# Performance work log

Measured on AMD Instinct MI355X. Metric: run time of the kernel, lower is better.

The kernel has to match this reference:

```python
import jax, jax.numpy as jnp
import numpy as np

WS = (14, 14)
NUM_HEADS = 12
DIM = 768
HEAD_DIM = DIM // NUM_HEADS
N_TOK = WS[0] * WS[1] + 1  # 197 (cls token)
NUM_REL = (2 * WS[0] - 1) * (2 * WS[1] - 1) + 3  # 732
B = 64


def _build_rel_pos_index():
    ch, cw = np.arange(WS[0]), np.arange(WS[1])
    coords = np.stack(np.meshgrid(ch, cw, indexing='ij'))  # [2,h,w]
    cf = coords.reshape(2, -1)  # [2, h*w]
    rel = cf[:, :, None] - cf[:, None, :]  # [2, hw, hw]
    rel = rel.transpose(1, 2, 0).astype(np.int64)
    rel[:, :, 0] += WS[0] - 1
    rel[:, :, 1] += WS[1] - 1
    rel[:, :, 0] *= 2 * WS[1] - 1
    idx = np.zeros((N_TOK, N_TOK), dtype=np.int64)
    idx[1:, 1:] = rel.sum(-1)
    idx[0, 0:] = NUM_REL - 3
    idx[0:, 0] = NUM_REL - 2
    idx[0, 0] = NUM_REL - 1
    return idx.astype(np.int32)


def setup_inputs() -> dict:
    key = jax.random.key(0)
    ks = jax.random.split(key, 7)
    s = 0.02
    return {
        'x': jax.random.normal(ks[0], (B, N_TOK, DIM), jnp.float32),
        'qkv_w': jax.random.normal(ks[1], (3 * DIM, DIM), jnp.float32) * s,
        'q_bias': jax.random.normal(ks[2], (DIM,), jnp.float32) * s,
        'v_bias': jax.random.normal(ks[3], (DIM,), jnp.float32) * s,
        'rpb_table': jax.random.normal(ks[4], (NUM_REL, NUM_HEADS), jnp.float32) * s,
        'proj_w': jax.random.normal(ks[5], (DIM, DIM), jnp.float32) * s,
        'proj_b': jax.random.normal(ks[6], (DIM,), jnp.float32) * s,
        'rel_pos_index': jnp.asarray(_build_rel_pos_index()),
    }


def reference(x, qkv_w, q_bias, v_bias, rpb_table, proj_w, proj_b, rel_pos_index):
    Bb, N, C = x.shape
    scale = HEAD_DIM ** -0.5
    # qkv bias: [q_bias, zeros(k), v_bias]
    qkv_bias = jnp.concatenate([q_bias, jnp.zeros_like(v_bias), v_bias])
    qkv = x @ qkv_w.T + qkv_bias  # [B,N,3C]
    qkv = qkv.reshape(Bb, N, 3, NUM_HEADS, HEAD_DIM).transpose(2, 0, 3, 1, 4)
    q, k, v = qkv[0], qkv[1], qkv[2]  # [B,H,N,hd]
    attn = jnp.einsum('bhnd,bhmd->bhnm', q * scale, k)
    # gather relative position bias: [N,N,H] -> [1,H,N,N]
    rpb = rpb_table[rel_pos_index]  # [N,N,H]
    attn = attn + rpb.transpose(2, 0, 1)[None]
    attn = jax.nn.softmax(attn, axis=-1)
    out = jnp.einsum('bhnm,bhmd->bhnd', attn, v)
    out = out.transpose(0, 2, 1, 3).reshape(Bb, N, NUM_HEADS * HEAD_DIM)
    return out @ proj_w.T + proj_b
```

## Files before the change

### kernel.cpp

```cpp
#include <hip/hip_runtime.h>
#include <hip/hip_bf16.h>
#include <cstdint>
#include <cstddef>

typedef __bf16 bf16x8 __attribute__((ext_vector_type(8)));
typedef float f32x4 __attribute__((ext_vector_type(4)));

#define DI __device__ __forceinline__
#define AS1 __attribute__((address_space(1)))
#define AS3 __attribute__((address_space(3)))

DI unsigned short f2bf(float x) {
    union { float f; unsigned int u; } v; v.f = x;
    unsigned int u = v.u;
    u += 0x7FFFu + ((u >> 16) & 1u);
    return (unsigned short)(u >> 16);
}

#define BATCH 64
#define NH 12
#define NTOK 197
#define NTOK_P 208
#define HD 64
#define DIM 768
#define MROWS 12608
#define MPAD 224
#define PLDS 232
#define CPAD 132
#define QSCALE 0.18033688f
#define LOG2E 1.4426950408889634f

DI int xcd_swz(int orig, int nwg) {
    int q = nwg >> 3, r = nwg & 7;
    int x = orig & 7, l = orig >> 3;
    return (x < r ? x * (q + 1) : r * (q + 1) + (x - r) * q) + l;
}

DI int swz(int row, int col_elem) {
    return (row * 64 + col_elem) ^ ((row & 7) << 3);
}


__global__ void cvt3_bf16_kernel(const float* __restrict__ a, unsigned short* __restrict__ oa, int na4,
                                 const float* __restrict__ b, unsigned short* __restrict__ ob, int nb4,
                                 const float* __restrict__ c, unsigned short* __restrict__ oc, int nc4) {
    int i = blockIdx.x * blockDim.x + threadIdx.x;
    const float* src; unsigned short* dst; int k;
    if (i < na4) { src = a; dst = oa; k = i; }
    else if (i < na4 + nb4) { src = b; dst = ob; k = i - na4; }
    else if (i < na4 + nb4 + nc4) { src = c; dst = oc; k = i - na4 - nb4; }
    else return;
    float4 f = ((const float4*)src)[k];
    ushort4 o;
    o.x = f2bf(f.x); o.y = f2bf(f.y); o.z = f2bf(f.z); o.w = f2bf(f.w);
    ((ushort4*)dst)[k] = o;
}

__global__ void build_rpb2_kernel(const float* __restrict__ table, const int* __restrict__ idx,
                                  float* __restrict__ out) {
    int i = blockIdx.x * blockDim.x + threadIdx.x;
    if (i >= NH * 13 * 13 * 256) return;
    int j = i & 3;
    int lane = (i >> 2) & 63;
    int t = (i >> 8) % 13;
    int qt = ((i >> 8) / 13) % 13;
    int h = (i >> 8) / 169;
    int row = qt * 16 + ((lane >> 4) << 2) + j;
    int col = t * 16 + (lane & 15);
    float v = 0.f;
    if (row < NTOK && col < NTOK) v = table[idx[row * NTOK + col] * NH + h] * LOG2E;
    out[i] = v;
}

__global__ void zero_vt_pad_kernel(unsigned short* __restrict__ vt) {
    const int npad = MPAD - NTOK;
    int i = blockIdx.x * blockDim.x + threadIdx.x;
    if (i >= BATCH * NH * HD * npad) return;
    int c = NTOK + (i % npad);
    int row = i / npad;
    vt[(size_t)row * MPAD + c] = 0;
}


template<int EPI>
__launch_bounds__(256)
__global__ void gemm_bt_kernel(const unsigned short* __restrict__ A,
                               const unsigned short* __restrict__ W,
                               const float* __restrict__ bias0,
                               const float* __restrict__ bias1,
                               void* __restrict__ out0,
                               unsigned short* __restrict__ out1,
                               unsigned short* __restrict__ out2,
                               int M, int ntiles)
{
    __shared__ __align__(16) unsigned short smem[32768];
    const int K = DIM;
    const int NT = K / 64;
    int wgid = xcd_swz(blockIdx.x, gridDim.x);
    int mt = wgid / ntiles, nt = wgid % ntiles;
    int m0 = mt * 128, n0 = nt * 128;
    int tid = threadIdx.x;
    int lane = tid & 63, w = tid >> 6;
    int wr = (w >> 1) * 64, wc = (w & 1) * 64;

    const int st_row = lane >> 3;
    const int st_col = ((lane & 7) ^ (lane >> 3)) << 3;

    f32x4 acc[4][4] = {};

    auto stage = [&](int buf, int ks) {
        unsigned short* as = smem + buf * 8192;
        unsigned short* bs = smem + 16384 + buf * 8192;
#pragma unroll
        for (int i = 0; i < 4; i++) {
            int s = w * 4 + i;
            int arow = m0 + s * 8 + st_row; if (arow >= M) arow = M - 1;
            __builtin_amdgcn_global_load_lds(
                (const AS1 void*)(A + (size_t)arow * K + ks + st_col),
                (AS3 void*)(as + s * 512), 16, 0, 0);
        }
#pragma unroll
        for (int i = 0; i < 4; i++) {
            int s = w * 4 + i;
            __builtin_amdgcn_global_load_lds(
                (const AS1 void*)(W + (size_t)(n0 + s * 8 + st_row) * K + ks + st_col),
                (AS3 void*)(bs + s * 512), 16, 0, 0);
        }
    };

    stage(0, 0);
    __syncthreads();
    int cur = 0;
    for (int t = 0; t < NT; ++t) {
        if (t + 1 < NT) stage(cur ^ 1, (t + 1) * 64);
        const unsigned short* as = smem + cur * 8192;
        const unsigned short* bs = smem + 16384 + cur * 8192;
#pragma unroll
        for (int kc = 0; kc < 2; kc++) {
            bf16x8 af[4], bfr[4];
#pragma unroll
            for (int x = 0; x < 4; x++)
                af[x] = *(const bf16x8*)&as[swz(wr + x * 16 + (lane & 15), kc * 32 + (lane >> 4) * 8)];
#pragma unroll
            for (int y = 0; y < 4; y++)
                bfr[y] = *(const bf16x8*)&bs[swz(wc + y * 16 + (lane & 15), kc * 32 + (lane >> 4) * 8)];
#pragma unroll
            for (int x = 0; x < 4; x++)
#pragma unroll
                for (int y = 0; y < 4; y++)
                    acc[x][y] = __builtin_amdgcn_mfma_f32_16x16x32_bf16(af[x], bfr[y], acc[x][y], 0, 0, 0);
        }
        __syncthreads();
        cur ^= 1;
    }

    if constexpr (EPI == 1) {
#pragma unroll
        for (int x = 0; x < 4; x++)
#pragma unroll
            for (int y = 0; y < 4; y++)
#pragma unroll
                for (int j = 0; j < 4; j++) {
                    int m = m0 + wr + x * 16 + (lane >> 4) * 4 + j;
                    int n = n0 + wc + y * 16 + (lane & 15);
                    if (m < M)
                        ((float*)out0)[(size_t)m * DIM + n] = acc[x][y][j] + bias0[n];
                }
    } else {
        int which = n0 / DIM;
        int hn0 = n0 - which * DIM;
        unsigned short* lc = smem;

#pragma unroll
        for (int x = 0; x < 4; x++)
#pragma unroll
            for (int y = 0; y < 4; y++)
#pragma unroll
                for (int j = 0; j < 4; j++) {
                    int ml = wr + x * 16 + (lane >> 4) * 4 + j;
                    int nl = wc + y * 16 + (lane & 15);
                    float val = acc[x][y][j];
                    if (which == 0) val = (val + bias0[hn0 + nl]) * QSCALE;
                    else if (which == 2) val = val + bias1[hn0 + nl];
                    lc[ml * CPAD + nl] = f2bf(val);
                }
        __syncthreads();

        if (which != 2) {
            unsigned short* outq = (which == 0) ? (unsigned short*)out0 : out1;
            int c4 = (lane & 31) * 4;
            int h = (hn0 >> 6) + (c4 >> 6), d = c4 & 63;
            for (int it = 0; it < 16; ++it) {
                int r = it * 8 + w * 2 + (lane >> 5);
                int m = m0 + r;
                if (m >= M) continue;
                int b = m / NTOK, t = m - b * NTOK;
                ushort4 q4 = *(const ushort4*)&lc[r * CPAD + c4];
                *(ushort4*)&outq[(((size_t)b * NH + h) * NTOK_P + t) * HD + d] = q4;
            }
        } else {
            int mh = w >> 1, hs = w & 1;
            int h = (hn0 >> 6) + hs;
            int ml = mh * 64 + lane;
            int m = m0 + ml;
            if (m < M) {
                int b = m / NTOK, t = m - b * NTOK;
                unsigned short* vbase = out2 + (((size_t)b * NH + h) * HD) * MPAD + t;
#pragma unroll 8
                for (int d = 0; d < 64; ++d)
                    vbase[(size_t)d * MPAD] = lc[ml * CPAD + hs * 64 + d];
            }
        }
    }
}


__launch_bounds__(64)
__global__ void attn_kernel(const unsigned short* __restrict__ qbuf,
                            const unsigned short* __restrict__ kbuf,
                            const unsigned short* __restrict__ vt,
                            const float* __restrict__ rpb2,
                            unsigned short* __restrict__ ao)
{
    __shared__ __align__(16) unsigned short p_lds[16][PLDS];
    int bid = xcd_swz(blockIdx.x, gridDim.x);
    int qt = bid % 13, bh = bid / 13;
    int b = bh / NH, h = bh - b * NH;
    int lane = threadIdx.x;
    int r0 = qt * 16;
    int col_l = lane & 15, hi = lane >> 4;

    {
        int rr = lane >> 2, cc = NTOK_P + (lane & 3) * 4;
        ushort4 z = {0, 0, 0, 0};
        *(ushort4*)&p_lds[rr][cc] = z;
    }

    const size_t kqbase = (size_t)bh * NTOK_P * HD;
    int qrow = r0 + col_l;
    bf16x8 qf0 = *(const bf16x8*)&qbuf[kqbase + (size_t)qrow * HD + hi * 8];
    bf16x8 qf1 = *(const bf16x8*)&qbuf[kqbase + (size_t)qrow * HD + 32 + hi * 8];

    const float* rpbase = rpb2 + (((size_t)(h * 13 + qt) * 13) << 8) + (lane << 2);

    float lrow[4] = {0.f, 0.f, 0.f, 0.f};
#pragma unroll
    for (int t = 0; t < 13; t++) {
        int krow = t * 16 + col_l;
        bf16x8 kf0 = *(const bf16x8*)&kbuf[kqbase + (size_t)krow * HD + hi * 8];
        bf16x8 kf1 = *(const bf16x8*)&kbuf[kqbase + (size_t)krow * HD + 32 + hi * 8];
        f32x4 z = {0.f, 0.f, 0.f, 0.f};
        f32x4 a = __builtin_amdgcn_mfma_f32_16x16x32_bf16(qf0, kf0, z, 0, 0, 0);
        f32x4 s = __builtin_amdgcn_mfma_f32_16x16x32_bf16(qf1, kf1, a, 0, 0, 0);
        float4 rb = *(const float4*)&rpbase[t << 8];
        float rbj[4] = {rb.x, rb.y, rb.z, rb.w};
        bool masked = (t * 16 + col_l >= NTOK);
#pragma unroll
        for (int j = 0; j < 4; j++) {
            float v = s[j] + rbj[j];
            if (masked) v = -1e30f;
            float p = exp2f(v);
            lrow[j] += p;
            p_lds[hi * 4 + j][t * 16 + col_l] = f2bf(p);
        }
    }
#pragma unroll
    for (int j = 0; j < 4; j++) {
        float lv = lrow[j];
        lv += __shfl_xor(lv, 1);
        lv += __shfl_xor(lv, 2);
        lv += __shfl_xor(lv, 4);
        lv += __shfl_xor(lv, 8);
        lrow[j] = lv;
    }
    float inv[4];
#pragma unroll
    for (int j = 0; j < 4; j++)
        inv[j] = __builtin_amdgcn_rcpf(lrow[j]);

    f32x4 o[4] = {};
    const size_t vbase = (size_t)bh * HD * MPAD;
    __builtin_amdgcn_s_setprio(1);
#pragma unroll
    for (int c = 0; c < 7; c++) {
        bf16x8 pf = *(const bf16x8*)&p_lds[col_l][c * 32 + hi * 8];
#pragma unroll
        for (int n = 0; n < 4; n++) {
            bf16x8 vf = *(const bf16x8*)&vt[vbase + (size_t)(n * 16 + col_l) * MPAD + c * 32 + hi * 8];
            o[n] = __builtin_amdgcn_mfma_f32_16x16x32_bf16(pf, vf, o[n], 0, 0, 0);
        }
    }
    __builtin_amdgcn_s_setprio(0);

    int rbase = r0 + hi * 4;
#pragma unroll
    for (int n = 0; n < 4; n++)
#pragma unroll
        for (int j = 0; j < 4; j++) {
            int tok = rbase + j;
            if (tok < NTOK) {
                float val = o[n][j] * inv[j];
                ao[((size_t)b * NTOK + tok) * DIM + h * HD + n * 16 + col_l] = f2bf(val);
            }
        }
}


extern "C" void kernel_launch(void* const* d_in, const int* in_sizes, int n_in,
                              void* d_out, int out_size, void* d_ws, size_t ws_size,
                              hipStream_t stream)
{
    const float* x      = (const float*)d_in[0];
    const float* qkv_w  = (const float*)d_in[1];
    const float* q_bias = (const float*)d_in[2];
    const float* v_bias = (const float*)d_in[3];
    const float* rpb_t  = (const float*)d_in[4];
    const float* proj_w = (const float*)d_in[5];
    const float* proj_b = (const float*)d_in[6];
    const int*   relidx = (const int*)d_in[7];
    float* out = (float*)d_out;

    char* ws = (char*)d_ws;
    const size_t SZ_XBF  = (size_t)MROWS * DIM * 2;
    const size_t SZ_QKVW = (size_t)3 * DIM * DIM * 2;
    const size_t SZ_PRJW = (size_t)DIM * DIM * 2;
    const size_t SZ_QK   = (size_t)BATCH * NH * NTOK_P * HD * 2;
    const size_t SZ_VT   = (size_t)BATCH * NH * HD * MPAD * 2;

    unsigned short* x_bf = (unsigned short*)ws;
    unsigned short* ao   = x_bf;
    size_t off = SZ_XBF;
    unsigned short* qkvw_bf  = (unsigned short*)(ws + off); off += SZ_QKVW;
    unsigned short* projw_bf = (unsigned short*)(ws + off); off += SZ_PRJW;
    unsigned short* qbuf     = (unsigned short*)(ws + off); off += SZ_QK;
    unsigned short* kbuf     = (unsigned short*)(ws + off); off += SZ_QK;
    unsigned short* vtbuf    = (unsigned short*)(ws + off); off += SZ_VT;
    float* rpbf              = (float*)(ws + off);

    const int NA4 = MROWS * DIM / 4, NB4 = 3 * DIM * DIM / 4, NC4 = DIM * DIM / 4;
    cvt3_bf16_kernel<<<(NA4 + NB4 + NC4 + 255) / 256, 256, 0, stream>>>(
        x, x_bf, NA4, qkv_w, qkvw_bf, NB4, proj_w, projw_bf, NC4);
    build_rpb2_kernel<<<(NH * 13 * 13 * 256 + 255) / 256, 256, 0, stream>>>(rpb_t, relidx, rpbf);
    zero_vt_pad_kernel<<<(BATCH * NH * HD * (MPAD - NTOK) + 255) / 256, 256, 0, stream>>>(vtbuf);

    gemm_bt_kernel<0><<<99 * 18, 256, 0, stream>>>(x_bf, qkvw_bf, q_bias, v_bias,
                                                   (void*)qbuf, kbuf, vtbuf, MROWS, 18);
    attn_kernel<<<BATCH * NH * 13, 64, 0, stream>>>(qbuf, kbuf, vtbuf, rpbf, ao);
    gemm_bt_kernel<1><<<99 * 6, 256, 0, stream>>>(ao, projw_bf, proj_b, nullptr,
                                                  (void*)out, nullptr, nullptr, MROWS, 6);
    (void)in_sizes; (void)n_in; (void)out_size; (void)ws_size;
}
```

Baseline: 194.1 us.

## Process two 16-row query tiles per attention wave to reuse K/V loads

Each attention block now handles 32 query rows (two 16-row MFMA groups) instead of 16, so each K and V fragment loaded from global memory feeds two MFMAs. The grid shrinks from 13 to 7 query tiles per head, and the relative-position-bias layout and its build kernel are reorganized to match. The goal is to halve redundant K/V global traffic and per-block overhead, at the cost of more registers and LDS per wave, fewer blocks, and some wasted work on the clamped last tile (rows 208–223).

Result: faster. 185.3 us (-4.5%).

```diff
diff --git a/kernel.cpp b/kernel.cpp
--- a/kernel.cpp
+++ b/kernel.cpp
@@ -25,7 +25,7 @@
 #define DIM 768
 #define MROWS 12608
 #define MPAD 224
-#define PLDS 232
+#define PLDS2 236
 #define CPAD 132
 #define QSCALE 0.18033688f
 #define LOG2E 1.4426950408889634f
@@ -59,13 +59,15 @@
 __global__ void build_rpb2_kernel(const float* __restrict__ table, const int* __restrict__ idx,
                                   float* __restrict__ out) {
     int i = blockIdx.x * blockDim.x + threadIdx.x;
-    if (i >= NH * 13 * 13 * 256) return;
+    if (i >= NH * 7 * 13 * 512) return;
     int j = i & 3;
-    int lane = (i >> 2) & 63;
-    int t = (i >> 8) % 13;
-    int qt = ((i >> 8) / 13) % 13;
-    int h = (i >> 8) / 169;
-    int row = qt * 16 + ((lane >> 4) << 2) + j;
+    int g = (i >> 2) & 1;
+    int lane = (i >> 3) & 63;
+    int rest = i >> 9;
+    int t = rest % 13;
+    int qt = (rest / 13) % 7;
+    int h = rest / 91;
+    int row = qt * 32 + g * 16 + ((lane >> 4) << 2) + j;
     int col = t * 16 + (lane & 15);
     float v = 0.f;
     if (row < NTOK && col < NTOK) v = table[idx[row * NTOK + col] * NH + h] * LOG2E;
@@ -222,87 +224,101 @@
                             const float* __restrict__ rpb2,
                             unsigned short* __restrict__ ao)
 {
-    __shared__ __align__(16) unsigned short p_lds[16][PLDS];
+    __shared__ __align__(16) unsigned short p_lds[32][PLDS2];
     int bid = xcd_swz(blockIdx.x, gridDim.x);
-    int qt = bid % 13, bh = bid / 13;
+    int qt = bid % 7, bh = bid / 7;
     int b = bh / NH, h = bh - b * NH;
     int lane = threadIdx.x;
-    int r0 = qt * 16;
+    int r0 = qt * 32;
     int col_l = lane & 15, hi = lane >> 4;
 
     {
-        int rr = lane >> 2, cc = NTOK_P + (lane & 3) * 4;
+        int rr = lane >> 1, cc = NTOK_P + (lane & 1) * 8;
         ushort4 z = {0, 0, 0, 0};
         *(ushort4*)&p_lds[rr][cc] = z;
+        *(ushort4*)&p_lds[rr][cc + 4] = z;
     }
 
     const size_t kqbase = (size_t)bh * NTOK_P * HD;
-    int qrow = r0 + col_l;
-    bf16x8 qf0 = *(const bf16x8*)&qbuf[kqbase + (size_t)qrow * HD + hi * 8];
-    bf16x8 qf1 = *(const bf16x8*)&qbuf[kqbase + (size_t)qrow * HD + 32 + hi * 8];
-
-    const float* rpbase = rpb2 + (((size_t)(h * 13 + qt) * 13) << 8) + (lane << 2);
-
-    float lrow[4] = {0.f, 0.f, 0.f, 0.f};
+    int qr0 = r0 + col_l;      if (qr0 > NTOK_P - 1) qr0 = NTOK_P - 1;
+    int qr1 = r0 + 16 + col_l; if (qr1 > NTOK_P - 1) qr1 = NTOK_P - 1;
+    bf16x8 qf0a = *(const bf16x8*)&qbuf[kqbase + (size_t)qr0 * HD + hi * 8];
+    bf16x8 qf0b = *(const bf16x8*)&qbuf[kqbase + (size_t)qr0 * HD + 32 + hi * 8];
+    bf16x8 qf1a = *(const bf16x8*)&qbuf[kqbase + (size_t)qr1 * HD + hi * 8];
+    bf16x8 qf1b = *(const bf16x8*)&qbuf[kqbase + (size_t)qr1 * HD + 32 + hi * 8];
+
+    const float* rpbase = rpb2 + ((size_t)(h * 7 + qt) * 13) * 512 + lane * 8;
+
+    float lrow[2][4] = {};
 #pragma unroll
     for (int t = 0; t < 13; t++) {
         int krow = t * 16 + col_l;
         bf16x8 kf0 = *(const bf16x8*)&kbuf[kqbase + (size_t)krow * HD + hi * 8];
         bf16x8 kf1 = *(const bf16x8*)&kbuf[kqbase + (size_t)krow * HD + 32 + hi * 8];
         f32x4 z = {0.f, 0.f, 0.f, 0.f};
-        f32x4 a = __builtin_amdgcn_mfma_f32_16x16x32_bf16(qf0, kf0, z, 0, 0, 0);
-        f32x4 s = __builtin_amdgcn_mfma_f32_16x16x32_bf16(qf1, kf1, a, 0, 0, 0);
-        float4 rb = *(const float4*)&rpbase[t << 8];
+        f32x4 sA = __builtin_amdgcn_mfma_f32_16x16x32_bf16(qf0a, kf0, z, 0, 0, 0);
+        sA = __builtin_amdgcn_mfma_f32_16x16x32_bf16(qf0b, kf1, sA, 0, 0, 0);
+        f32x4 sB = __builtin_amdgcn_mfma_f32_16x16x32_bf16(qf1a, kf0, z, 0, 0, 0);
+        sB = __builtin_amdgcn_mfma_f32_16x16x32_bf16(qf1b, kf1, sB, 0, 0, 0);
+        float4 ra = *(const float4*)&rpbase[(size_t)t * 512];
+        float4 rb = *(const float4*)&rpbase[(size_t)t * 512 + 4];
+        float raj[4] = {ra.x, ra.y, ra.z, ra.w};
         float rbj[4] = {rb.x, rb.y, rb.z, rb.w};
         bool masked = (t * 16 + col_l >= NTOK);
 #pragma unroll
         for (int j = 0; j < 4; j++) {
-            float v = s[j] + rbj[j];
-            if (masked) v = -1e30f;
-            float p = exp2f(v);
-            lrow[j] += p;
-            p_lds[hi * 4 + j][t * 16 + col_l] = f2bf(p);
-        }
-    }
-#pragma unroll
-    for (int j = 0; j < 4; j++) {
-        float lv = lrow[j];
-        lv += __shfl_xor(lv, 1);
-        lv += __shfl_xor(lv, 2);
-        lv += __shfl_xor(lv, 4);
-        lv += __shfl_xor(lv, 8);
-        lrow[j] = lv;
-    }
-    float inv[4];
-#pragma unroll
-    for (int j = 0; j < 4; j++)
-        inv[j] = __builtin_amdgcn_rcpf(lrow[j]);
-
-    f32x4 o[4] = {};
+            float vA = sA[j] + raj[j];
+            float vB = sB[j] + rbj[j];
+            if (masked) { vA = -1e30f; vB = -1e30f; }
+            float pA = exp2f(vA);
+            float pB = exp2f(vB);
+            lrow[0][j] += pA;
+            lrow[1][j] += pB;
+            p_lds[hi * 4 + j][t * 16 + col_l] = f2bf(pA);
+            p_lds[16 + hi * 4 + j][t * 16 + col_l] = f2bf(pB);
+        }
+    }
+    float inv[2][4];
+#pragma unroll
+    for (int g = 0; g < 2; g++)
+#pragma unroll
+        for (int j = 0; j < 4; j++) {
+            float lv = lrow[g][j];
+            lv += __shfl_xor(lv, 1);
+            lv += __shfl_xor(lv, 2);
+            lv += __shfl_xor(lv, 4);
+            lv += __shfl_xor(lv, 8);
+            inv[g][j] = __builtin_amdgcn_rcpf(lv);
+        }
+
+    f32x4 o[2][4] = {};
     const size_t vbase = (size_t)bh * HD * MPAD;
     __builtin_amdgcn_s_setprio(1);
 #pragma unroll
     for (int c = 0; c < 7; c++) {
-        bf16x8 pf = *(const bf16x8*)&p_lds[col_l][c * 32 + hi * 8];
+        bf16x8 pf0 = *(const bf16x8*)&p_lds[col_l][c * 32 + hi * 8];
+        bf16x8 pf1 = *(const bf16x8*)&p_lds[16 + col_l][c * 32 + hi * 8];
 #pragma unroll
         for (int n = 0; n < 4; n++) {
             bf16x8 vf = *(const bf16x8*)&vt[vbase + (size_t)(n * 16 + col_l) * MPAD + c * 32 + hi * 8];
-            o[n] = __builtin_amdgcn_mfma_f32_16x16x32_bf16(pf, vf, o[n], 0, 0, 0);
+            o[0][n] = __builtin_amdgcn_mfma_f32_16x16x32_bf16(pf0, vf, o[0][n], 0, 0, 0);
+            o[1][n] = __builtin_amdgcn_mfma_f32_16x16x32_bf16(pf1, vf, o[1][n], 0, 0, 0);
         }
     }
     __builtin_amdgcn_s_setprio(0);
 
-    int rbase = r0 + hi * 4;
-#pragma unroll
-    for (int n = 0; n < 4; n++)
-#pragma unroll
-        for (int j = 0; j < 4; j++) {
-            int tok = rbase + j;
-            if (tok < NTOK) {
-                float val = o[n][j] * inv[j];
-                ao[((size_t)b * NTOK + tok) * DIM + h * HD + n * 16 + col_l] = f2bf(val);
+#pragma unroll
+    for (int g = 0; g < 2; g++)
+#pragma unroll
+        for (int n = 0; n < 4; n++)
+#pragma unroll
+            for (int j = 0; j < 4; j++) {
+                int tok = r0 + g * 16 + hi * 4 + j;
+                if (tok < NTOK) {
+                    float val = o[g][n][j] * inv[g][j];
+                    ao[((size_t)b * NTOK + tok) * DIM + h * HD + n * 16 + col_l] = f2bf(val);
+                }
             }
-        }
 }
 
 
@@ -340,12 +356,12 @@
     const int NA4 = MROWS * DIM / 4, NB4 = 3 * DIM * DIM / 4, NC4 = DIM * DIM / 4;
     cvt3_bf16_kernel<<<(NA4 + NB4 + NC4 + 255) / 256, 256, 0, stream>>>(
         x, x_bf, NA4, qkv_w, qkvw_bf, NB4, proj_w, projw_bf, NC4);
-    build_rpb2_kernel<<<(NH * 13 * 13 * 256 + 255) / 256, 256, 0, stream>>>(rpb_t, relidx, rpbf);
+    build_rpb2_kernel<<<(NH * 7 * 13 * 512 + 255) / 256, 256, 0, stream>>>(rpb_t, relidx, rpbf);
     zero_vt_pad_kernel<<<(BATCH * NH * HD * (MPAD - NTOK) + 255) / 256, 256, 0, stream>>>(vtbuf);
 
     gemm_bt_kernel<0><<<99 * 18, 256, 0, stream>>>(x_bf, qkvw_bf, q_bias, v_bias,
                                                    (void*)qbuf, kbuf, vtbuf, MROWS, 18);
-    attn_kernel<<<BATCH * NH * 13, 64, 0, stream>>>(qbuf, kbuf, vtbuf, rpbf, ao);
+    attn_kernel<<<BATCH * NH * 7, 64, 0, stream>>>(qbuf, kbuf, vtbuf, rpbf, ao);
     gemm_bt_kernel<1><<<99 * 6, 256, 0, stream>>>(ao, projw_bf, proj_b, nullptr,
                                                   (void*)out, nullptr, nullptr, MROWS, 6);
     (void)in_sizes; (void)n_in; (void)out_size; (void)ws_size;
```
